# Kernel optimization log

Hardware: AMD Instinct MI355X
Metric: run time of the kernel (lower is better)

## Reference

```python
import jax, jax.numpy as jnp
import numpy as np

B, S, D = 4, 2048, 2048
E = 8            # num_experts
TOP_K = 2
H = 1408         # intermediate_size per expert
SH = 2 * H       # shared expert intermediate (shared_experts=2)


def setup_inputs() -> dict:
    key = jax.random.key(0)
    ks = jax.random.split(key, 8)
    sc = 0.02
    return {
        "hidden_states": jax.random.normal(ks[0], (B, S, D), jnp.float32),
        "gate_w": jax.random.normal(ks[1], (E, D), jnp.float32) * sc,   # torch Linear weight [out,in]
        "w1": jax.random.normal(ks[2], (E, H, D), jnp.float32) * sc,    # gate_proj per expert
        "w3": jax.random.normal(ks[3], (E, H, D), jnp.float32) * sc,    # up_proj per expert
        "w2": jax.random.normal(ks[4], (E, D, H), jnp.float32) * sc,    # down_proj per expert
        "sw1": jax.random.normal(ks[5], (SH, D), jnp.float32) * sc,
        "sw3": jax.random.normal(ks[6], (SH, D), jnp.float32) * sc,
        "sw2": jax.random.normal(ks[7], (D, SH), jnp.float32) * sc,
    }


def reference(hidden_states, gate_w, w1, w3, w2, sw1, sw3, sw2):
    b, s, d = hidden_states.shape
    x = hidden_states.reshape(-1, d)                      # [T, D]
    logits = x @ gate_w.T                                 # [T, E]
    rw, sel = jax.lax.top_k(logits, TOP_K)                # [T, K]
    rw = jax.nn.softmax(rw, axis=-1)                      # norm_topk_prob=True
    onehot = jax.nn.one_hot(sel, E, dtype=x.dtype)        # [T, K, E]
    token_mask = onehot.sum(axis=1)                       # [T, E] in {0,1}
    # NOTE: faithful to the source quirk: expert_weights.sum(dim=-1) on a flat
    # masked gather sums routing weights over ALL tokens selecting the expert,
    # producing one scalar per expert.
    s_e = (rw[..., None] * onehot).sum(axis=(0, 1))       # [E]
    combine = token_mask * s_e                            # [T, E]
    # per-expert SwiGLU MLP on all tokens (dense combine form of gather/scatter)
    g = jnp.einsum('td,ehd->eth', x, w1)                  # [E, T, H]
    u = jnp.einsum('td,ehd->eth', x, w3)
    a = jax.nn.silu(g) * u
    y = jnp.einsum('eth,edh->etd', a, w2)                 # [E, T, D]
    out = jnp.einsum('te,etd->td', combine, y)            # [T, D]
    shared = (jax.nn.silu(x @ sw1.T) * (x @ sw3.T)) @ sw2.T
    out = out + shared
    return out.reshape(b, s, d)
```

## Files before the change

kernel.cpp:

```cpp
#include <hip/hip_runtime.h>
#include <hip/hip_bf16.h>
#include <stdint.h>

#define T_TOK 8192
#define DIM   2048
#define NEXP  8
#define HDIM  1408
#define SHDIM 2816

typedef __attribute__((ext_vector_type(8))) short bfrag;
typedef __attribute__((ext_vector_type(4))) float f32x4;
typedef __attribute__((ext_vector_type(4))) short s16x4;

__device__ __forceinline__ short f2bf(float f) {
    union { float f; uint32_t u; } v; v.f = f;
    return (short)((v.u + 0x8000u) >> 16);
}
__device__ __forceinline__ float bf2f(short s) {
    union { uint32_t u; float f; } v; v.u = ((uint32_t)(uint16_t)s) << 16;
    return v.f;
}

__device__ __forceinline__ bfrag cvt8(float4 a, float4 b) {
    bfrag r;
    r[0] = f2bf(a.x); r[1] = f2bf(a.y); r[2] = f2bf(a.z); r[3] = f2bf(a.w);
    r[4] = f2bf(b.x); r[5] = f2bf(b.y); r[6] = f2bf(b.z); r[7] = f2bf(b.w);
    return r;
}

__device__ __forceinline__ void gload16(const void* g, void* l) {
    __builtin_amdgcn_global_load_lds(
        (__attribute__((address_space(1))) void*)(g),
        (__attribute__((address_space(3))) void*)(l), 16, 0, 0);
}

#define MFMA16(a, b, c) __builtin_amdgcn_mfma_f32_16x16x32_bf16((a), (b), (c), 0, 0, 0)


__global__ __launch_bounds__(256) void gate_cvt_kernel(
    const float* __restrict__ x, const float* __restrict__ gw,
    __hip_bfloat16* __restrict__ xbf,
    int* __restrict__ sel, int* __restrict__ meta, float* __restrict__ s_e,
    const float* __restrict__ sw1f, const float* __restrict__ sw3f,
    __hip_bfloat16* __restrict__ sw1bf, __hip_bfloat16* __restrict__ sw3bf)
{
    const int bid = blockIdx.x;
    if (bid >= T_TOK / 32) {
        constexpr size_t E_SW = (size_t)SHDIM * DIM;
        constexpr int NCH = (int)(2 * E_SW / 2048);
        const int w = bid - T_TOK / 32;
        for (int c = w; c < NCH; c += 256) {
            size_t elem = (size_t)c * 2048 + threadIdx.x * 8;
            const float* s; __hip_bfloat16* d;
            if (elem < E_SW) { s = sw1f + elem; d = sw1bf + elem; }
            else             { s = sw3f + (elem - E_SW); d = sw3bf + (elem - E_SW); }
            float4 a = ((const float4*)s)[0], b = ((const float4*)s)[1];
            *(bfrag*)d = cvt8(a, b);
        }
        return;
    }
    __shared__ float g[NEXP * DIM];
    for (int i = threadIdx.x; i < NEXP * DIM; i += 256) g[i] = gw[i];
    __syncthreads();
    const int wid = threadIdx.x >> 6, lane = threadIdx.x & 63;
    for (int it = 0; it < 8; ++it) {
        const int t = bid * 32 + wid * 8 + it;
        float acc[NEXP];
#pragma unroll
        for (int e = 0; e < NEXP; ++e) acc[e] = 0.f;
        const float4* xr = (const float4*)(x + (size_t)t * DIM);
        for (int j = 0; j < DIM / 4; j += 64) {
            float4 xv = xr[j + lane];
            s16x4 xv16 = { f2bf(xv.x), f2bf(xv.y), f2bf(xv.z), f2bf(xv.w) };
            *(s16x4*)&xbf[(size_t)t * DIM + (j + lane) * 4] = xv16;
#pragma unroll
            for (int e = 0; e < NEXP; ++e) {
                float4 gv = *(const float4*)&g[e * DIM + (j + lane) * 4];
                acc[e] += xv.x * gv.x + xv.y * gv.y + xv.z * gv.z + xv.w * gv.w;
            }
        }
#pragma unroll
        for (int e = 0; e < NEXP; ++e)
            for (int o = 32; o; o >>= 1) acc[e] += __shfl_xor(acc[e], o);
        if (lane == 0) {
            int e0 = 0; float v0 = acc[0];
#pragma unroll
            for (int e = 1; e < NEXP; ++e) if (acc[e] > v0) { v0 = acc[e]; e0 = e; }
            int e1 = -1; float v1 = -3.4e38f;
#pragma unroll
            for (int e = 0; e < NEXP; ++e) if (e != e0 && acc[e] > v1) { v1 = acc[e]; e1 = e; }
            float p0 = 1.f / (1.f + __expf(v1 - v0));
            float p1 = 1.f - p0;
            sel[2 * t] = e0; sel[2 * t + 1] = e1;
            atomicAdd(&s_e[e0], p0); atomicAdd(&s_e[e1], p1);
            atomicAdd(&meta[e0], 1); atomicAdd(&meta[e1], 1);
        }
    }
}

__global__ void scan_kernel(int* meta) {
    if (threadIdx.x == 0) {
        int acc = 0;
        for (int e = 0; e < NEXP; ++e) {
            meta[16 + e] = acc;
            meta[8 + e]  = acc;
            acc += meta[e];
        }
        meta[24] = acc;
    }
}

__global__ __launch_bounds__(256) void fill_kernel(
    const int* __restrict__ sel, int* __restrict__ meta,
    int* __restrict__ list, int2* __restrict__ slots)
{
    const int t = blockIdx.x * 256 + threadIdx.x;
    int e0 = sel[2 * t], e1 = sel[2 * t + 1];
    int p0 = atomicAdd(&meta[8 + e0], 1); list[p0] = t;
    int p1 = atomicAdd(&meta[8 + e1], 1); list[p1] = t;
    slots[t] = make_int2(p0, p1);
}


template<int N, bool GATHER>
__device__ __forceinline__ void up_core(
    const __hip_bfloat16* __restrict__ X,
    const __hip_bfloat16* __restrict__ B1p,
    const __hip_bfloat16* __restrict__ B3p,
    __hip_bfloat16* __restrict__ actp,
    const int* __restrict__ list,
    int base, int count, int m0, int n0, short* lds)
{
    constexpr int K = DIM;
    constexpr int NT = K / 64;
    short (*As)[256 * 64]  = (short (*)[256 * 64])lds;
    short (*B1s)[128 * 64] = (short (*)[128 * 64])(lds + 32768);
    short (*B3s)[128 * 64] = (short (*)[128 * 64])(lds + 49152);

    const int tid = threadIdx.x, wid = tid >> 6, lane = tid & 63;
    const int rlo = lane >> 3;
    const int swslot = (lane & 7) ^ rlo;

    const __hip_bfloat16* pA[4];
#pragma unroll
    for (int q = 0; q < 4; ++q) {
        int row = (q * 8 + wid) * 8 + rlo;
        int r = m0 + row; if (r > count - 1) r = count - 1;
        int ga = GATHER ? list[base + r] : r;
        pA[q] = X + (size_t)ga * K + swslot * 8;
    }
    const __hip_bfloat16* pB1[2];
    const __hip_bfloat16* pB3[2];
#pragma unroll
    for (int q = 0; q < 2; ++q) {
        int row = (q * 8 + wid) * 8 + rlo;
        pB1[q] = B1p + (size_t)(n0 + row) * K + swslot * 8;
        pB3[q] = B3p + (size_t)(n0 + row) * K + swslot * 8;
    }

#define STAGE_UP(T, BUF) do { const int k0_ = (T) * 64;                         \
    _Pragma("unroll") for (int q = 0; q < 4; ++q)                               \
        gload16(pA[q] + k0_, &As[BUF][(q * 8 + wid) * 512]);                    \
    _Pragma("unroll") for (int q = 0; q < 2; ++q) {                             \
        gload16(pB1[q] + k0_, &B1s[BUF][(q * 8 + wid) * 512]);                  \
        gload16(pB3[q] + k0_, &B3s[BUF][(q * 8 + wid) * 512]); } } while (0)

    const int wm = wid >> 2, wn = wid & 3;
    const int l15 = lane & 15, lhi = lane >> 4;

    f32x4 accg[8][2], accu[8][2];
#pragma unroll
    for (int i = 0; i < 8; ++i)
#pragma unroll
        for (int j = 0; j < 2; ++j) { accg[i][j] = 0.f; accu[i][j] = 0.f; }

    STAGE_UP(0, 0);
    __syncthreads();
    int cur = 0;
#pragma unroll 1
    for (int t = 0; t < NT; ++t) {
        if (t + 1 < NT) STAGE_UP(t + 1, cur ^ 1);
        __builtin_amdgcn_sched_barrier(0);
        bfrag b1f[2][2], b3f[2][2];
#pragma unroll
        for (int j = 0; j < 2; ++j)
#pragma unroll
            for (int kk = 0; kk < 2; ++kk) {
                int rb = wn * 32 + j * 16 + l15;
                int c = kk * 4 + lhi;
                int off = rb * 128 + ((c ^ (rb & 7)) << 4);
                b1f[j][kk] = *(const bfrag*)((const char*)B1s[cur] + off);
                b3f[j][kk] = *(const bfrag*)((const char*)B3s[cur] + off);
            }
        __builtin_amdgcn_s_setprio(1);
#pragma unroll
        for (int i = 0; i < 8; ++i) {
            int ra = wm * 128 + i * 16 + l15;
            const char* abase = (const char*)As[cur] + ra * 128;
            bfrag a0 = *(const bfrag*)(abase + ((lhi       ^ (ra & 7)) << 4));
            bfrag a1 = *(const bfrag*)(abase + (((4 + lhi) ^ (ra & 7)) << 4));
#pragma unroll
            for (int j = 0; j < 2; ++j) {
                accg[i][j] = MFMA16(a0, b1f[j][0], accg[i][j]);
                accu[i][j] = MFMA16(a0, b3f[j][0], accu[i][j]);
                accg[i][j] = MFMA16(a1, b1f[j][1], accg[i][j]);
                accu[i][j] = MFMA16(a1, b3f[j][1], accu[i][j]);
            }
        }
        __builtin_amdgcn_s_setprio(0);
        __syncthreads();
        cur ^= 1;
    }
#undef STAGE_UP

#pragma unroll
    for (int i = 0; i < 8; ++i)
#pragma unroll
        for (int r = 0; r < 4; ++r) {
            int m = wm * 128 + i * 16 + lhi * 4 + r;
            if (m0 + m < count) {
#pragma unroll
                for (int j = 0; j < 2; ++j) {
                    float gg = accg[i][j][r];
                    float uu = accu[i][j][r];
                    float a = gg / (1.f + __expf(-gg)) * uu;
                    int n = n0 + wn * 32 + j * 16 + l15;
                    actp[(size_t)(base + m0 + m) * N + n] = __float2bfloat16(a);
                }
            }
        }
}

template<int KD, bool TO_BF16>
__device__ __forceinline__ void down_core(
    const __hip_bfloat16* __restrict__ Ap,
    const __hip_bfloat16* __restrict__ Bp,
    float* __restrict__ out, __hip_bfloat16* __restrict__ yscr,
    int base, int count, int m0, int n0, short* lds)
{
    constexpr int NT = KD / 64;
    short (*As)[256 * 64] = (short (*)[256 * 64])lds;
    short (*Bs)[256 * 64] = (short (*)[256 * 64])(lds + 32768);

    const int tid = threadIdx.x, wid = tid >> 6, lane = tid & 63;
    const int rlo = lane >> 3;
    const int swslot = (lane & 7) ^ rlo;

    const __hip_bfloat16* pA[4];
    const __hip_bfloat16* pB[4];
#pragma unroll
    for (int q = 0; q < 4; ++q) {
        int row = (q * 8 + wid) * 8 + rlo;
        int r = m0 + row; if (r > count - 1) r = count - 1;
        pA[q] = Ap + (size_t)(base + r) * KD + swslot * 8;
        pB[q] = Bp + (size_t)(n0 + row) * KD + swslot * 8;
    }

#define STAGE_DN(T, BUF) do { const int k0_ = (T) * 64;                         \
    _Pragma("unroll") for (int q = 0; q < 4; ++q) {                             \
        gload16(pA[q] + k0_, &As[BUF][(q * 8 + wid) * 512]);                    \
        gload16(pB[q] + k0_, &Bs[BUF][(q * 8 + wid) * 512]); } } while (0)

    const int wm = wid >> 2, wn = wid & 3;
    const int l15 = lane & 15, lhi = lane >> 4;

    f32x4 acc[8][4];
#pragma unroll
    for (int i = 0; i < 8; ++i)
#pragma unroll
        for (int j = 0; j < 4; ++j) acc[i][j] = 0.f;

    STAGE_DN(0, 0);
    __syncthreads();
    int cur = 0;
#pragma unroll 1
    for (int t = 0; t < NT; ++t) {
        if (t + 1 < NT) STAGE_DN(t + 1, cur ^ 1);
        __builtin_amdgcn_sched_barrier(0);
        bfrag bf[4][2];
#pragma unroll
        for (int j = 0; j < 4; ++j)
#pragma unroll
            for (int kk = 0; kk < 2; ++kk) {
                int rb = wn * 64 + j * 16 + l15;
                int c = kk * 4 + lhi;
                bf[j][kk] = *(const bfrag*)((const char*)Bs[cur] + rb * 128 + ((c ^ (rb & 7)) << 4));
            }
        __builtin_amdgcn_s_setprio(1);
#pragma unroll
        for (int i = 0; i < 8; ++i) {
            int ra = wm * 128 + i * 16 + l15;
            const char* abase = (const char*)As[cur] + ra * 128;
            bfrag a0 = *(const bfrag*)(abase + ((lhi       ^ (ra & 7)) << 4));
            bfrag a1 = *(const bfrag*)(abase + (((4 + lhi) ^ (ra & 7)) << 4));
#pragma unroll
            for (int j = 0; j < 4; ++j) {
                acc[i][j] = MFMA16(a0, bf[j][0], acc[i][j]);
                acc[i][j] = MFMA16(a1, bf[j][1], acc[i][j]);
            }
        }
        __builtin_amdgcn_s_setprio(0);
        __syncthreads();
        cur ^= 1;
    }
#undef STAGE_DN

#pragma unroll
    for (int i = 0; i < 8; ++i)
#pragma unroll
        for (int r = 0; r < 4; ++r) {
            int m = wm * 128 + i * 16 + lhi * 4 + r;
            if (m0 + m < count) {
#pragma unroll
                for (int j = 0; j < 4; ++j) {
                    int n = n0 + wn * 64 + j * 16 + l15;
                    if (TO_BF16)
                        yscr[(size_t)(base + m0 + m) * DIM + n] = __float2bfloat16(acc[i][j][r]);
                    else
                        out[(size_t)(m0 + m) * DIM + n] = acc[i][j][r];
                }
            }
        }
}

#define UPSH_NG 704
#define UPSH_NCVT 512
__global__ __launch_bounds__(512, 2) void upsh_cvt_k(
    const __hip_bfloat16* __restrict__ X,
    const __hip_bfloat16* __restrict__ SW1, const __hip_bfloat16* __restrict__ SW3,
    __hip_bfloat16* __restrict__ act_sh,
    const float* __restrict__ w1f, const float* __restrict__ w3f,
    const float* __restrict__ w2f, const float* __restrict__ sw2f,
    __hip_bfloat16* __restrict__ w1bf, __hip_bfloat16* __restrict__ w3bf,
    __hip_bfloat16* __restrict__ w2bf, __hip_bfloat16* __restrict__ sw2bf)
{
    const int bid = blockIdx.x;
    if (bid >= UPSH_NG) {
        constexpr size_t E_W  = (size_t)NEXP * HDIM * DIM;
        constexpr size_t E_SW = (size_t)SHDIM * DIM;
        constexpr int NCH = (int)((3 * E_W + E_SW) / 4096);
        const int w = bid - UPSH_NG;
        for (int c = w; c < NCH; c += UPSH_NCVT) {
            size_t elem = (size_t)c * 4096 + threadIdx.x * 8;
            const float* s; __hip_bfloat16* d;
            if      (elem < E_W)          { s = w1f + elem;               d = w1bf + elem; }
            else if (elem < 2 * E_W)      { s = w3f + (elem - E_W);       d = w3bf + (elem - E_W); }
            else if (elem < 3 * E_W)      { s = w2f + (elem - 2 * E_W);   d = w2bf + (elem - 2 * E_W); }
            else                          { s = sw2f + (elem - 3 * E_W);  d = sw2bf + (elem - 3 * E_W); }
            float4 a = ((const float4*)s)[0], b = ((const float4*)s)[1];
            *(bfrag*)d = cvt8(a, b);
        }
        return;
    }
    constexpr int nx = SHDIM / 128, cpx = UPSH_NG / 8;
    const int virt = (bid & 7) * cpx + (bid >> 3);
    const int xi = virt % nx, yi = virt / nx;
    __shared__ alignas(16) short lds[65536];
    up_core<SHDIM, false>(X, SW1, SW3, act_sh, nullptr, 0, T_TOK, yi * 256, xi * 128, lds);
}

template<int KD, bool TO_BF16>
__global__ __launch_bounds__(512, 2) void down_k(
    const __hip_bfloat16* __restrict__ A, const __hip_bfloat16* __restrict__ W2,
    float* __restrict__ out, __hip_bfloat16* __restrict__ yscr,
    const int* __restrict__ meta)
{
    constexpr int nx = DIM / 256, ny = T_TOK / 256, nz = TO_BF16 ? NEXP : 1;
    constexpr int nwg = nx * ny * nz, cpx = nwg / 8;
    const int bid = (int)blockIdx.x + nx * ((int)blockIdx.y + ny * (int)blockIdx.z);
    const int virt = (bid & 7) * cpx + (bid >> 3);
    const int xi = virt % nx, rest = virt / nx, yi = rest % ny, e = rest / ny;
    int count, base;
    if (TO_BF16) { count = meta[e]; base = meta[16 + e]; if (yi * 256 >= count) return; }
    else { count = T_TOK; base = 0; }
    __shared__ alignas(16) short lds[65536];
    down_core<KD, TO_BF16>(A, W2 + (size_t)e * DIM * KD, out, yscr,
                           base, count, yi * 256, xi * 256, lds);
}

template<int N, bool GATHER>
__global__ __launch_bounds__(512, 2) void up_k(
    const __hip_bfloat16* __restrict__ X,
    const __hip_bfloat16* __restrict__ W1, const __hip_bfloat16* __restrict__ W3,
    __hip_bfloat16* __restrict__ act,
    const int* __restrict__ list, const int* __restrict__ meta)
{
    constexpr int nx = N / 128, ny = T_TOK / 256, nz = GATHER ? NEXP : 1;
    constexpr int nwg = nx * ny * nz, cpx = nwg / 8;
    const int bid = (int)blockIdx.x + nx * ((int)blockIdx.y + ny * (int)blockIdx.z);
    const int virt = (bid & 7) * cpx + (bid >> 3);
    const int xi = virt % nx, rest = virt / nx, yi = rest % ny, e = rest / ny;
    int count, base;
    if (GATHER) { count = meta[e]; base = meta[16 + e]; if (yi * 256 >= count) return; }
    else { count = T_TOK; base = 0; }
    __shared__ alignas(16) short lds[65536];
    up_core<N, GATHER>(X, W1 + (size_t)e * N * DIM, W3 + (size_t)e * N * DIM,
                       act, list, base, count, yi * 256, xi * 128, lds);
}

__global__ __launch_bounds__(512, 2) void mid_merged(
    const __hip_bfloat16* __restrict__ act_sh, const __hip_bfloat16* __restrict__ sw2bf,
    float* __restrict__ out,
    const __hip_bfloat16* __restrict__ xbf,
    const __hip_bfloat16* __restrict__ w1bf, const __hip_bfloat16* __restrict__ w3bf,
    __hip_bfloat16* __restrict__ act_ex,
    const int* __restrict__ list, const int* __restrict__ meta)
{
    __shared__ alignas(16) short lds[65536];
    const int bid = (int)blockIdx.x;
    if (bid < 256) {
        constexpr int cpx = 256 / 8;
        const int virt = (bid & 7) * cpx + (bid >> 3);
        const int n0 = (virt & 7) * 256, m0 = (virt >> 3) * 256;
        down_core<SHDIM, false>(act_sh, sw2bf, out, nullptr, 0, T_TOK, m0, n0, lds);
    } else {
        const int b = bid - 256;
        constexpr int cpx = 2816 / 8;
        const int virt = (b & 7) * cpx + (b >> 3);
        const int e = virt / 352, r = virt % 352;
        const int n0 = (r % 11) * 128, m0 = (r / 11) * 256;
        const int count = meta[e], base = meta[16 + e];
        if (m0 >= count) return;
        up_core<HDIM, true>(xbf, w1bf + (size_t)e * HDIM * DIM, w3bf + (size_t)e * HDIM * DIM,
                            act_ex, list, base, count, m0, n0, lds);
    }
}

__global__ __launch_bounds__(256) void combine_kernel(
    float* __restrict__ out, const __hip_bfloat16* __restrict__ yscr,
    const int* __restrict__ sel, const int2* __restrict__ slots,
    const float* __restrict__ s_e)
{
    const int t = blockIdx.x;
    const int d = threadIdx.x * 8;
    const int2 sl = slots[t];
    const float se0 = s_e[sel[2 * t]];
    const float se1 = s_e[sel[2 * t + 1]];
    bfrag y0 = *(const bfrag*)&yscr[(size_t)sl.x * DIM + d];
    bfrag y1 = *(const bfrag*)&yscr[(size_t)sl.y * DIM + d];
    float4* o = (float4*)(out + (size_t)t * DIM + d);
    float4 o0 = o[0], o1 = o[1];
    o0.x += se0 * bf2f(y0[0]) + se1 * bf2f(y1[0]);
    o0.y += se0 * bf2f(y0[1]) + se1 * bf2f(y1[1]);
    o0.z += se0 * bf2f(y0[2]) + se1 * bf2f(y1[2]);
    o0.w += se0 * bf2f(y0[3]) + se1 * bf2f(y1[3]);
    o1.x += se0 * bf2f(y0[4]) + se1 * bf2f(y1[4]);
    o1.y += se0 * bf2f(y0[5]) + se1 * bf2f(y1[5]);
    o1.z += se0 * bf2f(y0[6]) + se1 * bf2f(y1[6]);
    o1.w += se0 * bf2f(y0[7]) + se1 * bf2f(y1[7]);
    o[0] = o0; o[1] = o1;
}

extern "C" void kernel_launch(void* const* d_in, const int* in_sizes, int n_in,
                              void* d_out, int out_size, void* d_ws, size_t ws_size,
                              hipStream_t stream) {
    const float* x   = (const float*)d_in[0];
    const float* gw  = (const float*)d_in[1];
    const float* w1  = (const float*)d_in[2];
    const float* w3  = (const float*)d_in[3];
    const float* w2  = (const float*)d_in[4];
    const float* sw1 = (const float*)d_in[5];
    const float* sw3 = (const float*)d_in[6];
    const float* sw2 = (const float*)d_in[7];
    float* out = (float*)d_out;

    const size_t SZ_X    = (size_t)T_TOK * DIM * 2;
    const size_t SZ_W    = (size_t)NEXP * HDIM * DIM * 2;
    const size_t SZ_SW   = (size_t)SHDIM * DIM * 2;
    const size_t SZ_ACTS = (size_t)T_TOK * SHDIM * 2;
    const size_t SZ_ACTE = (size_t)2 * T_TOK * HDIM * 2;
    const size_t SZ_INTS = (size_t)6 * T_TOK * sizeof(int) + 512;
    const size_t need_base   = SZ_X + 3 * SZ_W + 3 * SZ_SW + SZ_ACTS + SZ_INTS;
    const size_t need_merged = need_base + SZ_ACTE;

    char* p = (char*)d_ws;
    __hip_bfloat16* xbf   = (__hip_bfloat16*)p; p += SZ_X;
    __hip_bfloat16* w1bf  = (__hip_bfloat16*)p; p += SZ_W;
    __hip_bfloat16* w3bf  = (__hip_bfloat16*)p; p += SZ_W;
    __hip_bfloat16* w2bf  = (__hip_bfloat16*)p; p += SZ_W;
    __hip_bfloat16* sw1bf = (__hip_bfloat16*)p; p += SZ_SW;
    __hip_bfloat16* sw3bf = (__hip_bfloat16*)p; p += SZ_SW;
    __hip_bfloat16* sw2bf = (__hip_bfloat16*)p; p += SZ_SW;
    __hip_bfloat16* act_sh = (__hip_bfloat16*)p; p += SZ_ACTS;
    const bool merged = (need_merged <= ws_size);
    __hip_bfloat16* act_ex = merged ? (__hip_bfloat16*)p : act_sh;
    if (merged) p += SZ_ACTE;
    int*  list  = (int*)p;  p += (size_t)2 * T_TOK * sizeof(int);
    int*  sel   = (int*)p;  p += (size_t)2 * T_TOK * sizeof(int);
    int2* slots = (int2*)p; p += (size_t)2 * T_TOK * sizeof(int);
    int*  meta  = (int*)p;
    float* s_e  = (float*)(meta + 32);
    __hip_bfloat16* yscr = (__hip_bfloat16*)d_ws;
    if (need_base > ws_size) return;

    hipMemsetAsync(meta, 0, 256, stream);
    gate_cvt_kernel<<<T_TOK / 32 + 256, 256, 0, stream>>>(
        x, gw, xbf, sel, meta, s_e, sw1, sw3, sw1bf, sw3bf);
    scan_kernel<<<1, 64, 0, stream>>>(meta);
    fill_kernel<<<T_TOK / 256, 256, 0, stream>>>(sel, meta, list, slots);

    upsh_cvt_k<<<UPSH_NG + UPSH_NCVT, 512, 0, stream>>>(
        xbf, sw1bf, sw3bf, act_sh, w1, w3, w2, sw2, w1bf, w3bf, w2bf, sw2bf);

    if (merged) {
        mid_merged<<<256 + 2816, 512, 0, stream>>>(
            act_sh, sw2bf, out, xbf, w1bf, w3bf, act_ex, list, meta);
        down_k<HDIM, true><<<dim3(DIM / 256, T_TOK / 256, NEXP), 512, 0, stream>>>(
            act_ex, w2bf, out, yscr, meta);
    } else {
        down_k<SHDIM, false><<<dim3(DIM / 256, T_TOK / 256, 1), 512, 0, stream>>>(
            act_sh, sw2bf, out, nullptr, meta);
        up_k<HDIM, true><<<dim3(HDIM / 128, T_TOK / 256, NEXP), 512, 0, stream>>>(
            xbf, w1bf, w3bf, act_ex, list, meta);
        down_k<HDIM, true><<<dim3(DIM / 256, T_TOK / 256, NEXP), 512, 0, stream>>>(
            act_ex, w2bf, out, yscr, meta);
    }
    combine_kernel<<<T_TOK, 256, 0, stream>>>(out, yscr, sel, slots, s_e);
}
```

Before: 987.8 us.

## Redistribute fp32-to-bf16 weight conversion across kernels to overlap with GEMMs

Moves the sw2 conversion into the gate kernel and the w2 conversion into the mid_merged kernel as extra trailing blocks. The upsh kernel now converts only w1 and w3, with fewer conversion blocks. The aim is to spread the memory-bound conversion work so it runs alongside compute-bound GEMM blocks in each stage, rather than piling up in one kernel. A standalone w2 conversion kernel is added for the non-merged path. The added blocks in mid_merged delay its tail, and LDS is now declared after an early-return branch.

Result: faster. 963.9 us (-2.4%).

```diff
diff --git a/kernel.cpp b/kernel.cpp
--- a/kernel.cpp
+++ b/kernel.cpp
@@ -42,18 +42,21 @@
     __hip_bfloat16* __restrict__ xbf,
     int* __restrict__ sel, int* __restrict__ meta, float* __restrict__ s_e,
     const float* __restrict__ sw1f, const float* __restrict__ sw3f,
-    __hip_bfloat16* __restrict__ sw1bf, __hip_bfloat16* __restrict__ sw3bf)
+    const float* __restrict__ sw2f,
+    __hip_bfloat16* __restrict__ sw1bf, __hip_bfloat16* __restrict__ sw3bf,
+    __hip_bfloat16* __restrict__ sw2bf)
 {
     const int bid = blockIdx.x;
     if (bid >= T_TOK / 32) {
         constexpr size_t E_SW = (size_t)SHDIM * DIM;
-        constexpr int NCH = (int)(2 * E_SW / 2048);
+        constexpr int NCH = (int)(3 * E_SW / 2048);
         const int w = bid - T_TOK / 32;
         for (int c = w; c < NCH; c += 256) {
             size_t elem = (size_t)c * 2048 + threadIdx.x * 8;
             const float* s; __hip_bfloat16* d;
-            if (elem < E_SW) { s = sw1f + elem; d = sw1bf + elem; }
-            else             { s = sw3f + (elem - E_SW); d = sw3bf + (elem - E_SW); }
+            if      (elem < E_SW)     { s = sw1f + elem;             d = sw1bf + elem; }
+            else if (elem < 2 * E_SW) { s = sw3f + (elem - E_SW);    d = sw3bf + (elem - E_SW); }
+            else                      { s = sw2f + (elem - 2 * E_SW); d = sw2bf + (elem - 2 * E_SW); }
             float4 a = ((const float4*)s)[0], b = ((const float4*)s)[1];
             *(bfrag*)d = cvt8(a, b);
         }
@@ -324,29 +327,24 @@
 }
 
 #define UPSH_NG 704
-#define UPSH_NCVT 512
+#define UPSH_NCVT 384
 __global__ __launch_bounds__(512, 2) void upsh_cvt_k(
     const __hip_bfloat16* __restrict__ X,
     const __hip_bfloat16* __restrict__ SW1, const __hip_bfloat16* __restrict__ SW3,
     __hip_bfloat16* __restrict__ act_sh,
     const float* __restrict__ w1f, const float* __restrict__ w3f,
-    const float* __restrict__ w2f, const float* __restrict__ sw2f,
-    __hip_bfloat16* __restrict__ w1bf, __hip_bfloat16* __restrict__ w3bf,
-    __hip_bfloat16* __restrict__ w2bf, __hip_bfloat16* __restrict__ sw2bf)
+    __hip_bfloat16* __restrict__ w1bf, __hip_bfloat16* __restrict__ w3bf)
 {
     const int bid = blockIdx.x;
     if (bid >= UPSH_NG) {
-        constexpr size_t E_W  = (size_t)NEXP * HDIM * DIM;
-        constexpr size_t E_SW = (size_t)SHDIM * DIM;
-        constexpr int NCH = (int)((3 * E_W + E_SW) / 4096);
+        constexpr size_t E_W = (size_t)NEXP * HDIM * DIM;
+        constexpr int NCH = (int)(2 * E_W / 4096);
         const int w = bid - UPSH_NG;
         for (int c = w; c < NCH; c += UPSH_NCVT) {
             size_t elem = (size_t)c * 4096 + threadIdx.x * 8;
             const float* s; __hip_bfloat16* d;
-            if      (elem < E_W)          { s = w1f + elem;               d = w1bf + elem; }
-            else if (elem < 2 * E_W)      { s = w3f + (elem - E_W);       d = w3bf + (elem - E_W); }
-            else if (elem < 3 * E_W)      { s = w2f + (elem - 2 * E_W);   d = w2bf + (elem - 2 * E_W); }
-            else                          { s = sw2f + (elem - 3 * E_W);  d = sw2bf + (elem - 3 * E_W); }
+            if (elem < E_W) { s = w1f + elem;         d = w1bf + elem; }
+            else            { s = w3f + (elem - E_W); d = w3bf + (elem - E_W); }
             float4 a = ((const float4*)s)[0], b = ((const float4*)s)[1];
             *(bfrag*)d = cvt8(a, b);
         }
@@ -398,24 +396,52 @@
                        act, list, base, count, yi * 256, xi * 128, lds);
 }
 
+__global__ __launch_bounds__(256) void cvt_w2_kernel(
+    const float* __restrict__ w2f, __hip_bfloat16* __restrict__ w2bf)
+{
+    constexpr size_t E_W = (size_t)NEXP * HDIM * DIM;
+    const int stride = gridDim.x * 256;
+    for (size_t i = blockIdx.x * 256 + threadIdx.x; i < E_W / 8; i += stride) {
+        const float4* p = (const float4*)(w2f + i * 8);
+        float4 a = p[0], b = p[1];
+        *(bfrag*)(w2bf + i * 8) = cvt8(a, b);
+    }
+}
+
+#define MID_NDS 256
+#define MID_NUE 2816
+#define MID_NCVT 256
 __global__ __launch_bounds__(512, 2) void mid_merged(
     const __hip_bfloat16* __restrict__ act_sh, const __hip_bfloat16* __restrict__ sw2bf,
     float* __restrict__ out,
     const __hip_bfloat16* __restrict__ xbf,
     const __hip_bfloat16* __restrict__ w1bf, const __hip_bfloat16* __restrict__ w3bf,
     __hip_bfloat16* __restrict__ act_ex,
-    const int* __restrict__ list, const int* __restrict__ meta)
-{
+    const int* __restrict__ list, const int* __restrict__ meta,
+    const float* __restrict__ w2f, __hip_bfloat16* __restrict__ w2bf)
+{
+    const int bid = (int)blockIdx.x;
+    if (bid >= MID_NDS + MID_NUE) {
+        constexpr size_t E_W = (size_t)NEXP * HDIM * DIM;
+        constexpr int NCH = (int)(E_W / 4096);
+        const int w = bid - (MID_NDS + MID_NUE);
+        for (int c = w; c < NCH; c += MID_NCVT) {
+            size_t elem = (size_t)c * 4096 + threadIdx.x * 8;
+            float4 a = ((const float4*)(w2f + elem))[0];
+            float4 b = ((const float4*)(w2f + elem))[1];
+            *(bfrag*)(w2bf + elem) = cvt8(a, b);
+        }
+        return;
+    }
     __shared__ alignas(16) short lds[65536];
-    const int bid = (int)blockIdx.x;
-    if (bid < 256) {
-        constexpr int cpx = 256 / 8;
+    if (bid < MID_NDS) {
+        constexpr int cpx = MID_NDS / 8;
         const int virt = (bid & 7) * cpx + (bid >> 3);
         const int n0 = (virt & 7) * 256, m0 = (virt >> 3) * 256;
         down_core<SHDIM, false>(act_sh, sw2bf, out, nullptr, 0, T_TOK, m0, n0, lds);
     } else {
-        const int b = bid - 256;
-        constexpr int cpx = 2816 / 8;
+        const int b = bid - MID_NDS;
+        constexpr int cpx = MID_NUE / 8;
         const int virt = (b & 7) * cpx + (b >> 3);
         const int e = virt / 352, r = virt % 352;
         const int n0 = (r % 11) * 128, m0 = (r / 11) * 256;
@@ -495,19 +521,20 @@
 
     hipMemsetAsync(meta, 0, 256, stream);
     gate_cvt_kernel<<<T_TOK / 32 + 256, 256, 0, stream>>>(
-        x, gw, xbf, sel, meta, s_e, sw1, sw3, sw1bf, sw3bf);
+        x, gw, xbf, sel, meta, s_e, sw1, sw3, sw2, sw1bf, sw3bf, sw2bf);
     scan_kernel<<<1, 64, 0, stream>>>(meta);
     fill_kernel<<<T_TOK / 256, 256, 0, stream>>>(sel, meta, list, slots);
 
     upsh_cvt_k<<<UPSH_NG + UPSH_NCVT, 512, 0, stream>>>(
-        xbf, sw1bf, sw3bf, act_sh, w1, w3, w2, sw2, w1bf, w3bf, w2bf, sw2bf);
+        xbf, sw1bf, sw3bf, act_sh, w1, w3, w1bf, w3bf);
 
     if (merged) {
-        mid_merged<<<256 + 2816, 512, 0, stream>>>(
-            act_sh, sw2bf, out, xbf, w1bf, w3bf, act_ex, list, meta);
+        mid_merged<<<MID_NDS + MID_NUE + MID_NCVT, 512, 0, stream>>>(
+            act_sh, sw2bf, out, xbf, w1bf, w3bf, act_ex, list, meta, w2, w2bf);
         down_k<HDIM, true><<<dim3(DIM / 256, T_TOK / 256, NEXP), 512, 0, stream>>>(
             act_ex, w2bf, out, yscr, meta);
     } else {
+        cvt_w2_kernel<<<2048, 256, 0, stream>>>(w2, w2bf);
         down_k<SHDIM, false><<<dim3(DIM / 256, T_TOK / 256, 1), 512, 0, stream>>>(
             act_sh, sw2bf, out, nullptr, meta);
         up_k<HDIM, true><<<dim3(HDIM / 128, T_TOK / 256, NEXP), 512, 0, stream>>>(
```
